# Optimization experiments

Hardware: AMD Instinct MI355X
Metric: run time of the kernel (lower is better)

## Reference

```python
import jax, jax.numpy as jnp
import numpy as np

B, N, D, K = 128, 512, 512, 8

def setup_inputs() -> dict:
    key = jax.random.key(0)
    ks = jax.random.split(key, 6)
    coefficients = jax.random.normal(ks[0], (B, N, D), dtype=jnp.float32)
    H = D // 2
    s1 = 1.0 / np.sqrt(D)
    s2 = 1.0 / np.sqrt(H)
    W1 = jax.random.uniform(ks[1], (D, H), jnp.float32, -s1, s1)
    b1 = jax.random.uniform(ks[2], (H,), jnp.float32, -s1, s1)
    W2 = jax.random.uniform(ks[3], (H,), jnp.float32, -s2, s2)
    b2 = jax.random.uniform(ks[4], (), jnp.float32, -s2, s2)
    base_logits = jnp.zeros((N,), jnp.float32)  # nn.Parameter(torch.zeros(n_freqs))
    return {"coefficients": coefficients, "W1": W1, "b1": b1, "W2": W2, "b2": b2,
            "base_logits": base_logits}

def reference(coefficients, W1, b1, W2, b2, base_logits):
    # scorer: Linear(D, D//2) -> GELU(exact) -> Linear(D//2, 1), squeeze last dim
    h = jax.nn.gelu(jnp.einsum('bnd,dh->bnh', coefficients, W1) + b1, approximate=False)
    logits = jnp.einsum('bnh,h->bn', h, W2) + b2 + base_logits[None, :]  # (B, N)
    # inference path (self.training == False): plain softmax, no gumbel noise
    probs = jax.nn.softmax(logits, axis=-1)
    _, indices = jax.lax.top_k(probs, K)                      # (B, K) int32
    mask = jnp.zeros_like(probs).at[jnp.arange(B)[:, None], indices].set(1.0)
    selected = jnp.take_along_axis(coefficients, indices[:, :, None], axis=1)  # (B, K, D)
    importance = probs  # softmax(logits) again in torch; identical in eval mode
    return selected, mask, importance, indices
```

## Files before the change

kernel.cpp:

```cpp
#include <hip/hip_runtime.h>
#include <math.h>

#define B_DIM 128
#define N_DIM 512
#define D_DIM 512
#define H_DIM 256
#define K_SEL 8

typedef _Float16 half8 __attribute__((ext_vector_type(8)));
typedef float    f32x4 __attribute__((ext_vector_type(4)));

__device__ __forceinline__ void gload_lds16(const void* g, void* l) {
    __builtin_amdgcn_global_load_lds((const __attribute__((address_space(1))) void*)g,
                                     (__attribute__((address_space(3))) void*)l, 16, 0, 0);
}

__global__ __launch_bounds__(512) void prep_w1_kernel(
    const float* __restrict__ W1,
    _Float16* __restrict__ w1frag_h,
    _Float16* __restrict__ w1frag_l)
{
    const int b    = blockIdx.x;
    const int c4   = b >> 4;
    const int ks   = b & 15;
    const int lane = threadIdx.x >> 3;
    const int j    = threadIdx.x & 7;
    const int col  = c4 * 16 + (lane & 15);
    const int k    = ks * 32 + (lane >> 4) * 8 + j;
    float x = W1[(size_t)k * H_DIM + col];
    _Float16 h = (_Float16)x;
    float r = x - (float)h;
    size_t o = (size_t)b * 512 + lane * 8 + j;
    w1frag_h[o] = h;
    w1frag_l[o] = (_Float16)(r * 2048.0f);
}

__global__ __launch_bounds__(512, 1) void fused_scorer_mfma(
    const float* __restrict__ X,
    const _Float16* __restrict__ w1frag_h,
    const _Float16* __restrict__ w1frag_l,
    const float* __restrict__ b1,
    const float* __restrict__ W2,
    float* __restrict__ lp)
{
    __shared__ half8 Ah[2][1024], Al[2][1024];
    __shared__ half8 Bh[2][512],  Bl[2][512];

    const int tid  = threadIdx.x;
    const int lane = tid & 63;
    const int wave = tid >> 6;
    const int wm   = (wave >> 1) << 6;
    const int wnx  = wave & 1;
    const int l15  = lane & 15;
    const int lg   = lane >> 4;
    const int rowtile = blockIdx.x & 255;
    const int colhalf = blockIdx.x >> 8;
    const int row0 = rowtile * 256;

    const int rc  = tid & 255;
    const int kc1 = tid >> 8;
    const float* xp = X + (size_t)(row0 + rc) * D_DIM + kc1 * 8;

    const _Float16* bsrc_h = w1frag_h + ((size_t)(colhalf * 8 + (tid >> 6)) * 16) * 512 + (tid & 63) * 8;
    const _Float16* bsrc_l = w1frag_l + ((size_t)(colhalf * 8 + (tid >> 6)) * 16) * 512 + (tid & 63) * 8;

    f32x4 acc[4][4], acc2[4][4];
    #pragma unroll
    for (int mi = 0; mi < 4; ++mi)
        #pragma unroll
        for (int nj = 0; nj < 4; ++nj) {
            acc[mi][nj]  = (f32x4){0.f, 0.f, 0.f, 0.f};
            acc2[mi][nj] = (f32x4){0.f, 0.f, 0.f, 0.f};
        }

    float4 xv[4];
    auto load_a = [&](int k0) {
        xv[0] = *reinterpret_cast<const float4*>(xp + k0);
        xv[1] = *reinterpret_cast<const float4*>(xp + k0 + 4);
        xv[2] = *reinterpret_cast<const float4*>(xp + k0 + 16);
        xv[3] = *reinterpret_cast<const float4*>(xp + k0 + 20);
    };
    auto split_write = [&](int buf) {
        #pragma unroll
        for (int q = 0; q < 2; ++q) {
            float e[8] = {xv[2*q].x, xv[2*q].y, xv[2*q].z, xv[2*q].w,
                          xv[2*q+1].x, xv[2*q+1].y, xv[2*q+1].z, xv[2*q+1].w};
            half8 hh, ll;
            #pragma unroll
            for (int j = 0; j < 8; ++j) {
                _Float16 h = (_Float16)e[j];
                float r = e[j] - (float)h;
                hh[j] = h;
                ll[j] = (_Float16)(r * 2048.0f);
            }
            Ah[buf][tid + q * 512] = hh;
            Al[buf][tid + q * 512] = ll;
        }
    };
    auto stage_b = [&](int buf, int ks) {
        gload_lds16(bsrc_h + (size_t)ks * 512, &Bh[buf][tid]);
        gload_lds16(bsrc_l + (size_t)ks * 512, &Bl[buf][tid]);
    };

    load_a(0);
    stage_b(0, 0);
    split_write(0);
    load_a(32);
    __syncthreads();

    for (int ks = 0; ks < 16; ++ks) {
        const int buf = ks & 1, nbuf = buf ^ 1;
        if (ks < 15) {
            stage_b(nbuf, ks + 1);
            split_write(nbuf);
            if (ks < 14) load_a((ks + 2) * 32);
        }
        half8 fbh[4], fbl[4];
        #pragma unroll
        for (int nj = 0; nj < 4; ++nj) {
            int cb = (wnx * 4 + nj) * 64 + lane;
            fbh[nj] = Bh[buf][cb];
            fbl[nj] = Bl[buf][cb];
        }
        #pragma unroll
        for (int p = 0; p < 2; ++p) {
            half8 fah[2], fal[2];
            #pragma unroll
            for (int m = 0; m < 2; ++m) {
                int ca = lg * 256 + wm + (p * 2 + m) * 16 + l15;
                fah[m] = Ah[buf][ca];
                fal[m] = Al[buf][ca];
            }
            #pragma unroll
            for (int nj = 0; nj < 4; ++nj)
                #pragma unroll
                for (int m = 0; m < 2; ++m) {
                    int mi = p * 2 + m;
                    acc[mi][nj]  = __builtin_amdgcn_mfma_f32_16x16x32_f16(fah[m], fbh[nj], acc[mi][nj],  0, 0, 0);
                    acc2[mi][nj] = __builtin_amdgcn_mfma_f32_16x16x32_f16(fah[m], fbl[nj], acc2[mi][nj], 0, 0, 0);
                    acc2[mi][nj] = __builtin_amdgcn_mfma_f32_16x16x32_f16(fal[m], fbh[nj], acc2[mi][nj], 0, 0, 0);
                }
        }
        __syncthreads();
    }

    float b1v[4], w2v[4];
    #pragma unroll
    for (int nj = 0; nj < 4; ++nj) {
        int col = colhalf * 128 + wnx * 64 + nj * 16 + l15;
        b1v[nj] = b1[col];
        w2v[nj] = W2[col];
    }
    float part[4][4];
    #pragma unroll
    for (int mi = 0; mi < 4; ++mi)
        #pragma unroll
        for (int r = 0; r < 4; ++r)
            part[mi][r] = 0.f;
    #pragma unroll
    for (int mi = 0; mi < 4; ++mi)
        #pragma unroll
        for (int nj = 0; nj < 4; ++nj)
            #pragma unroll
            for (int r = 0; r < 4; ++r) {
                float z = acc[mi][nj][r] + acc2[mi][nj][r] * (1.0f / 2048.0f) + b1v[nj];
                float g = 0.5f * z * (1.0f + erff(z * 0.70710678118654752440f));
                part[mi][r] = fmaf(g, w2v[nj], part[mi][r]);
            }
    float* red = reinterpret_cast<float*>(&Ah[0][0]);
    #pragma unroll
    for (int mi = 0; mi < 4; ++mi)
        #pragma unroll
        for (int r = 0; r < 4; ++r) {
            float v = part[mi][r];
            v += __shfl_xor(v, 1, 16);
            v += __shfl_xor(v, 2, 16);
            v += __shfl_xor(v, 4, 16);
            v += __shfl_xor(v, 8, 16);
            if (l15 == 0)
                red[wnx * 256 + wm + mi * 16 + lg * 4 + r] = v;
        }
    __syncthreads();
    if (tid < 256)
        lp[(size_t)colhalf * 65536 + row0 + tid] = red[tid] + red[256 + tid];
}

__global__ __launch_bounds__(256) void softmax_topk_kernel(
    const float* __restrict__ lp,
    const float* __restrict__ b2p,
    const float* __restrict__ base_logits,
    float* __restrict__ out_mask,
    float* __restrict__ out_importance,
    float* __restrict__ out_indices)
{
    const int b = blockIdx.x;
    const int tid = threadIdx.x;
    __shared__ float probs[N_DIM];
    __shared__ float redf[4];
    __shared__ int   redi[4];
    __shared__ int   sel_idx[K_SEL];

    const float b2v = b2p[0];
    int i0g = b * N_DIM + tid;
    int i1g = i0g + 256;
    float l0 = lp[i0g] + lp[65536 + i0g] + b2v + base_logits[tid];
    float l1 = lp[i1g] + lp[65536 + i1g] + b2v + base_logits[tid + 256];

    float m = fmaxf(l0, l1);
    #pragma unroll
    for (int s = 32; s >= 1; s >>= 1) m = fmaxf(m, __shfl_xor(m, s, 64));
    if ((tid & 63) == 0) redf[tid >> 6] = m;
    __syncthreads();
    float gm = fmaxf(fmaxf(redf[0], redf[1]), fmaxf(redf[2], redf[3]));
    __syncthreads();

    float e0 = expf(l0 - gm), e1 = expf(l1 - gm);
    float ssum = e0 + e1;
    #pragma unroll
    for (int s = 32; s >= 1; s >>= 1) ssum += __shfl_xor(ssum, s, 64);
    if ((tid & 63) == 0) redf[tid >> 6] = ssum;
    __syncthreads();
    float denom = redf[0] + redf[1] + redf[2] + redf[3];
    float p0 = e0 / denom, p1 = e1 / denom;
    probs[tid] = p0;
    probs[tid + 256] = p1;
    out_importance[b * N_DIM + tid] = p0;
    out_importance[b * N_DIM + tid + 256] = p1;
    __syncthreads();

    for (int it = 0; it < K_SEL; ++it) {
        float v0 = probs[tid]; int i0 = tid;
        float v1 = probs[tid + 256];
        if (v1 > v0) { v0 = v1; i0 = tid + 256; }
        #pragma unroll
        for (int s = 32; s >= 1; s >>= 1) {
            float ov = __shfl_xor(v0, s, 64);
            int   oi = __shfl_xor(i0, s, 64);
            if (ov > v0 || (ov == v0 && oi < i0)) { v0 = ov; i0 = oi; }
        }
        if ((tid & 63) == 0) { redf[tid >> 6] = v0; redi[tid >> 6] = i0; }
        __syncthreads();
        if (tid == 0) {
            float bv = redf[0]; int bi = redi[0];
            for (int w = 1; w < 4; ++w)
                if (redf[w] > bv || (redf[w] == bv && redi[w] < bi)) { bv = redf[w]; bi = redi[w]; }
            sel_idx[it] = bi;
            probs[bi] = -1.0f;
        }
        __syncthreads();
    }

    float mk0 = 0.f, mk1 = 0.f;
    #pragma unroll
    for (int i = 0; i < K_SEL; ++i) {
        if (sel_idx[i] == tid)       mk0 = 1.f;
        if (sel_idx[i] == tid + 256) mk1 = 1.f;
    }
    out_mask[b * N_DIM + tid] = mk0;
    out_mask[b * N_DIM + tid + 256] = mk1;

    if (tid < K_SEL) out_indices[b * K_SEL + tid] = (float)sel_idx[tid];
}

__global__ __launch_bounds__(256) void gather_kernel(
    const float* __restrict__ X,
    const float* __restrict__ out_indices,
    float* __restrict__ out_selected)
{
    const int b = blockIdx.x;
    const int tid = threadIdx.x;
    __shared__ int sel[K_SEL];
    if (tid < K_SEL) sel[tid] = (int)out_indices[b * K_SEL + tid];
    __syncthreads();
    #pragma unroll
    for (int i = 0; i < 4; ++i) {
        int f = tid + 256 * i;
        int ki = f >> 7;
        int c4 = f & 127;
        float4 v = reinterpret_cast<const float4*>(
            X + ((size_t)b * N_DIM + sel[ki]) * D_DIM)[c4];
        reinterpret_cast<float4*>(
            out_selected + ((size_t)b * K_SEL + ki) * D_DIM)[c4] = v;
    }
}

extern "C" void kernel_launch(void* const* d_in, const int* in_sizes, int n_in,
                              void* d_out, int out_size, void* d_ws, size_t ws_size,
                              hipStream_t stream) {
    const float* X           = (const float*)d_in[0];
    const float* W1          = (const float*)d_in[1];
    const float* b1          = (const float*)d_in[2];
    const float* W2          = (const float*)d_in[3];
    const float* b2          = (const float*)d_in[4];
    const float* base_logits = (const float*)d_in[5];

    float* out            = (float*)d_out;
    float* out_selected   = out;
    float* out_mask       = out_selected + B_DIM * K_SEL * D_DIM;
    float* out_importance = out_mask + B_DIM * N_DIM;
    float* out_indices    = out_importance + B_DIM * N_DIM;

    float*    lp       = out_selected;
    _Float16* w1frag_h = (_Float16*)(out_selected + 131072);
    _Float16* w1frag_l = (_Float16*)(out_selected + 196608);

    hipLaunchKernelGGL(prep_w1_kernel, dim3(256), dim3(512), 0, stream,
                       W1, w1frag_h, w1frag_l);
    hipLaunchKernelGGL(fused_scorer_mfma, dim3(512), dim3(512), 0, stream,
                       X, w1frag_h, w1frag_l, b1, W2, lp);
    hipLaunchKernelGGL(softmax_topk_kernel, dim3(B_DIM), dim3(256), 0, stream,
                       lp, b2, base_logits, out_mask, out_importance, out_indices);
    hipLaunchKernelGGL(gather_kernel, dim3(B_DIM), dim3(256), 0, stream,
                       X, out_indices, out_selected);
}
```

Baseline: 110.9 us.

## Pre-split X into fp16 hi/lo fragments and use direct-load MFMA scorer

Adds a prep kernel that converts X into fp16 high/low fragments laid out in MFMA order in the workspace. A new scorer then has each wave own 16 rows and all 256 hidden columns, loading fragments straight from global memory with no LDS staging or cross-wave reduction. The bias, b2 and base logits are folded into the scorer, so the softmax kernel only reads final logits. This trades an extra full pass over X (a 128 MB fp32 read plus a 128 MB fp16 write) for a simpler, more occupant main GEMM. The old path is kept as a fallback for when the workspace is too small.

```diff
diff --git a/kernel.cpp b/kernel.cpp
--- a/kernel.cpp
+++ b/kernel.cpp
@@ -35,6 +35,101 @@
     w1frag_l[o] = (_Float16)(r * 2048.0f);
 }
 
+__global__ __launch_bounds__(512) void prep_x_kernel(
+    const float* __restrict__ X,
+    _Float16* __restrict__ xfrag_h,
+    _Float16* __restrict__ xfrag_l)
+{
+    const int rb   = blockIdx.x;
+    const int lane = threadIdx.x & 63;
+    const int ks8  = threadIdx.x >> 6;
+    const int row  = rb * 16 + (lane & 15);
+    const int lg   = lane >> 4;
+    #pragma unroll
+    for (int kk = 0; kk < 2; ++kk) {
+        int ks = ks8 + kk * 8;
+        const float* xp = X + (size_t)row * D_DIM + ks * 32 + lg * 8;
+        float4 a = *reinterpret_cast<const float4*>(xp);
+        float4 b = *reinterpret_cast<const float4*>(xp + 4);
+        float e[8] = {a.x, a.y, a.z, a.w, b.x, b.y, b.z, b.w};
+        half8 hh, ll;
+        #pragma unroll
+        for (int j = 0; j < 8; ++j) {
+            _Float16 h = (_Float16)e[j];
+            float r = e[j] - (float)h;
+            hh[j] = h;
+            ll[j] = (_Float16)(r * 2048.0f);
+        }
+        size_t o = ((size_t)rb * 16 + ks) * 512 + lane * 8;
+        *reinterpret_cast<half8*>(xfrag_h + o) = hh;
+        *reinterpret_cast<half8*>(xfrag_l + o) = ll;
+    }
+}
+
+__global__ __launch_bounds__(512, 2) void fused_scorer_direct(
+    const _Float16* __restrict__ xfrag_h,
+    const _Float16* __restrict__ xfrag_l,
+    const _Float16* __restrict__ w1frag_h,
+    const _Float16* __restrict__ w1frag_l,
+    const float* __restrict__ b1,
+    const float* __restrict__ W2,
+    const float* __restrict__ b2p,
+    const float* __restrict__ base_logits,
+    float* __restrict__ logits)
+{
+    const int lane = threadIdx.x & 63;
+    const int wave = threadIdx.x >> 6;
+    const int lg   = lane >> 4;
+    const int rb   = blockIdx.x * 8 + wave;
+
+    const _Float16* xph = xfrag_h + ((size_t)rb * 16) * 512 + lane * 8;
+    const _Float16* xpl = xfrag_l + ((size_t)rb * 16) * 512 + lane * 8;
+    const _Float16* wph = w1frag_h + lane * 8;
+    const _Float16* wpl = w1frag_l + lane * 8;
+
+    f32x4 acc[16];
+    #pragma unroll
+    for (int m = 0; m < 16; ++m) acc[m] = (f32x4){0.f, 0.f, 0.f, 0.f};
+    const f32x4 z4 = (f32x4){0.f, 0.f, 0.f, 0.f};
+
+    #pragma unroll 4
+    for (int ks = 0; ks < 16; ++ks) {
+        half8 axh = *reinterpret_cast<const half8*>(xph + ks * 512);
+        half8 axl = *reinterpret_cast<const half8*>(xpl + ks * 512);
+        #pragma unroll
+        for (int m = 0; m < 16; ++m) {
+            size_t wo = (size_t)(m * 16 + ks) * 512;
+            half8 wh = *reinterpret_cast<const half8*>(wph + wo);
+            half8 wl = *reinterpret_cast<const half8*>(wpl + wo);
+            acc[m] = __builtin_amdgcn_mfma_f32_16x16x32_f16(wh, axh, acc[m], 0, 0, 0);
+            f32x4 t = __builtin_amdgcn_mfma_f32_16x16x32_f16(wh, axl, z4, 0, 0, 0);
+            t = __builtin_amdgcn_mfma_f32_16x16x32_f16(wl, axh, t, 0, 0, 0);
+            acc[m] += t * (1.0f / 2048.0f);
+        }
+    }
+
+    float part = 0.f;
+    #pragma unroll
+    for (int m = 0; m < 16; ++m) {
+        float4 b1v = *reinterpret_cast<const float4*>(b1 + m * 16 + lg * 4);
+        float4 w2v = *reinterpret_cast<const float4*>(W2 + m * 16 + lg * 4);
+        float bb[4] = {b1v.x, b1v.y, b1v.z, b1v.w};
+        float ww[4] = {w2v.x, w2v.y, w2v.z, w2v.w};
+        #pragma unroll
+        for (int r = 0; r < 4; ++r) {
+            float z = acc[m][r] + bb[r];
+            float g = 0.5f * z * (1.0f + erff(z * 0.70710678118654752440f));
+            part = fmaf(g, ww[r], part);
+        }
+    }
+    part += __shfl_xor(part, 16, 64);
+    part += __shfl_xor(part, 32, 64);
+    if (lane < 16) {
+        int row = rb * 16 + lane;
+        logits[row] = part + b2p[0] + base_logits[row & (N_DIM - 1)];
+    }
+}
+
 __global__ __launch_bounds__(512, 1) void fused_scorer_mfma(
     const float* __restrict__ X,
     const _Float16* __restrict__ w1frag_h,
@@ -60,7 +155,6 @@
     const int rc  = tid & 255;
     const int kc1 = tid >> 8;
     const float* xp = X + (size_t)(row0 + rc) * D_DIM + kc1 * 8;
-
     const _Float16* bsrc_h = w1frag_h + ((size_t)(colhalf * 8 + (tid >> 6)) * 16) * 512 + (tid & 63) * 8;
     const _Float16* bsrc_l = w1frag_l + ((size_t)(colhalf * 8 + (tid >> 6)) * 16) * 512 + (tid & 63) * 8;
 
@@ -185,7 +279,79 @@
         lp[(size_t)colhalf * 65536 + row0 + tid] = red[tid] + red[256 + tid];
 }
 
-__global__ __launch_bounds__(256) void softmax_topk_kernel(
+__global__ __launch_bounds__(256) void softmax_topk_logits(
+    const float* __restrict__ logits,
+    float* __restrict__ out_mask,
+    float* __restrict__ out_importance,
+    float* __restrict__ out_indices)
+{
+    const int b = blockIdx.x;
+    const int tid = threadIdx.x;
+    __shared__ float probs[N_DIM];
+    __shared__ float redf[4];
+    __shared__ int   redi[4];
+    __shared__ int   sel_idx[K_SEL];
+
+    float l0 = logits[b * N_DIM + tid];
+    float l1 = logits[b * N_DIM + tid + 256];
+
+    float m = fmaxf(l0, l1);
+    #pragma unroll
+    for (int s = 32; s >= 1; s >>= 1) m = fmaxf(m, __shfl_xor(m, s, 64));
+    if ((tid & 63) == 0) redf[tid >> 6] = m;
+    __syncthreads();
+    float gm = fmaxf(fmaxf(redf[0], redf[1]), fmaxf(redf[2], redf[3]));
+    __syncthreads();
+
+    float e0 = expf(l0 - gm), e1 = expf(l1 - gm);
+    float ssum = e0 + e1;
+    #pragma unroll
+    for (int s = 32; s >= 1; s >>= 1) ssum += __shfl_xor(ssum, s, 64);
+    if ((tid & 63) == 0) redf[tid >> 6] = ssum;
+    __syncthreads();
+    float denom = redf[0] + redf[1] + redf[2] + redf[3];
+    float p0 = e0 / denom, p1 = e1 / denom;
+    probs[tid] = p0;
+    probs[tid + 256] = p1;
+    out_importance[b * N_DIM + tid] = p0;
+    out_importance[b * N_DIM + tid + 256] = p1;
+    __syncthreads();
+
+    for (int it = 0; it < K_SEL; ++it) {
+        float v0 = probs[tid]; int i0 = tid;
+        float v1 = probs[tid + 256];
+        if (v1 > v0) { v0 = v1; i0 = tid + 256; }
+        #pragma unroll
+        for (int s = 32; s >= 1; s >>= 1) {
+            float ov = __shfl_xor(v0, s, 64);
+            int   oi = __shfl_xor(i0, s, 64);
+            if (ov > v0 || (ov == v0 && oi < i0)) { v0 = ov; i0 = oi; }
+        }
+        if ((tid & 63) == 0) { redf[tid >> 6] = v0; redi[tid >> 6] = i0; }
+        __syncthreads();
+        if (tid == 0) {
+            float bv = redf[0]; int bi = redi[0];
+            for (int w = 1; w < 4; ++w)
+                if (redf[w] > bv || (redf[w] == bv && redi[w] < bi)) { bv = redf[w]; bi = redi[w]; }
+            sel_idx[it] = bi;
+            probs[bi] = -1.0f;
+        }
+        __syncthreads();
+    }
+
+    float mk0 = 0.f, mk1 = 0.f;
+    #pragma unroll
+    for (int i = 0; i < K_SEL; ++i) {
+        if (sel_idx[i] == tid)       mk0 = 1.f;
+        if (sel_idx[i] == tid + 256) mk1 = 1.f;
+    }
+    out_mask[b * N_DIM + tid] = mk0;
+    out_mask[b * N_DIM + tid + 256] = mk1;
+
+    if (tid < K_SEL) out_indices[b * K_SEL + tid] = (float)sel_idx[tid];
+}
+
+__global__ __launch_bounds__(256) void softmax_topk_lp(
     const float* __restrict__ lp,
     const float* __restrict__ b2p,
     const float* __restrict__ base_logits,
@@ -300,16 +466,34 @@
     float* out_importance = out_mask + B_DIM * N_DIM;
     float* out_indices    = out_importance + B_DIM * N_DIM;
 
-    float*    lp       = out_selected;
     _Float16* w1frag_h = (_Float16*)(out_selected + 131072);
     _Float16* w1frag_l = (_Float16*)(out_selected + 196608);
 
     hipLaunchKernelGGL(prep_w1_kernel, dim3(256), dim3(512), 0, stream,
                        W1, w1frag_h, w1frag_l);
-    hipLaunchKernelGGL(fused_scorer_mfma, dim3(512), dim3(512), 0, stream,
-                       X, w1frag_h, w1frag_l, b1, W2, lp);
-    hipLaunchKernelGGL(softmax_topk_kernel, dim3(B_DIM), dim3(256), 0, stream,
-                       lp, b2, base_logits, out_mask, out_importance, out_indices);
+
+    const size_t XFRAG_ELEMS = (size_t)65536 * 512;
+    const size_t WS_NEEDED   = XFRAG_ELEMS * 2 * sizeof(_Float16);
+
+    if (ws_size >= WS_NEEDED) {
+        _Float16* xfrag_h = (_Float16*)d_ws;
+        _Float16* xfrag_l = xfrag_h + XFRAG_ELEMS;
+        float* logits = out_selected;
+        hipLaunchKernelGGL(prep_x_kernel, dim3(4096), dim3(512), 0, stream,
+                           X, xfrag_h, xfrag_l);
+        hipLaunchKernelGGL(fused_scorer_direct, dim3(512), dim3(512), 0, stream,
+                           xfrag_h, xfrag_l, w1frag_h, w1frag_l,
+                           b1, W2, b2, base_logits, logits);
+        hipLaunchKernelGGL(softmax_topk_logits, dim3(B_DIM), dim3(256), 0, stream,
+                           logits, out_mask, out_importance, out_indices);
+    } else {
+        float* lp = out_selected;
+        hipLaunchKernelGGL(fused_scorer_mfma, dim3(512), dim3(512), 0, stream,
+                           X, w1frag_h, w1frag_l, b1, W2, lp);
+        hipLaunchKernelGGL(softmax_topk_lp, dim3(B_DIM), dim3(256), 0, stream,
+                           lp, b2, base_logits, out_mask, out_importance, out_indices);
+    }
+
     hipLaunchKernelGGL(gather_kernel, dim3(B_DIM), dim3(256), 0, stream,
                        X, out_indices, out_selected);
 }
```

Result: slower. 251.3 us (+126.6%).
